# Optimization experiments

Hardware: AMD Instinct MI355X
Metric: run time of the kernel (lower is better)

## Reference

```python
import jax, jax.numpy as jnp
import numpy as np

N_DYADIC = 0  # dyadic refinement order 'n' from SigLoss_MMD.__init__


def _sig_gram(X, Y, n):
    """Gram matrix of signature kernels k(x_i, y_j) via the first-order
    finite-difference PDE scheme used by sig_kernels_f/fb_mmd:
        K[i+1,j+1] = K[i+1,j] + K[i,j+1] + K[i,j]*(<dx_i, dy_j> - 1)
    with dyadically refined increments dx = (x_{t+1}-x_t)/2^n repeated 2^n times.
    X: (A, M, D), Y: (B, N, D) -> returns (A, B) = K[:, :, -1, -1].
    The row recurrence is a cumulative sum, so each PDE row is one cumsum
    (fully vectorized over all (A,B) pairs); lax.scan runs over rows.
    """
    f = 2 ** n
    incX = jnp.repeat((X[:, 1:] - X[:, :-1]) / f, f, axis=1)  # (A, MM, D)
    incY = jnp.repeat((Y[:, 1:] - Y[:, :-1]) / f, f, axis=1)  # (B, NN, D)
    Mmat = jnp.einsum('aid,bjd->abij', incX, incY)            # (A, B, MM, NN)
    A, B, MM, NN = Mmat.shape
    ones_col = jnp.ones((A, B, 1), Mmat.dtype)
    row0 = jnp.ones((A, B, NN + 1), Mmat.dtype)               # K[0, :] = 1

    def step(prev_row, Mrow):  # prev_row: (A,B,NN+1), Mrow: (A,B,NN)
        # K[i+1,j+1] - K[i+1,j] = K[i,j+1] + K[i,j]*(M[i,j]-1)  -> cumsum
        inc = prev_row[..., 1:] + prev_row[..., :-1] * (Mrow - 1.0)
        new_row = jnp.concatenate([ones_col, 1.0 + jnp.cumsum(inc, axis=-1)], axis=-1)
        return new_row, None

    last_row, _ = jax.lax.scan(step, row0, jnp.moveaxis(Mmat, 2, 0))
    return last_row[..., -1]  # (A, B)


def setup_inputs() -> dict:
    key = jax.random.key(0)
    kx, ky = jax.random.split(key)
    A, M, D = 64, 128, 128
    SCALE = 0.025  # keeps increment inner products small so the PDE stays bounded
    X = SCALE * jax.random.normal(kx, (A, M, D), dtype=jnp.float32)
    Y = SCALE * jax.random.normal(ky, (A, M, D), dtype=jnp.float32)
    return {"X": X, "Y": Y}


def reference(X, Y):
    K_XX = _sig_gram(X, X, N_DYADIC)
    K_YY = _sig_gram(Y, Y, N_DYADIC)
    K_XY = _sig_gram(X, Y, N_DYADIC)
    mmd_squared = jnp.mean(K_XX) + jnp.mean(K_YY) - 2.0 * jnp.mean(K_XY)
    return mmd_squared
```

## Files before the change

### kernel.cpp

```cpp
#include <hip/hip_runtime.h>
#include <hip/hip_bf16.h>

#define MM 127
#define CHUNK_U16 4096
#define MAT_U16   16384
#define ARR_U16   1048576
#define QS_STRIDE 136
#define QS_DWORDS (64 * QS_STRIDE)

typedef __attribute__((ext_vector_type(8))) short short8;
typedef __attribute__((ext_vector_type(4))) float floatx4;

__device__ __forceinline__ unsigned short f2bf_rne(float x) {
  unsigned int u = __float_as_uint(x);
  u += 0x7FFFu + ((u >> 16) & 1u);
  return (unsigned short)(u >> 16);
}

__device__ __forceinline__ void gload_lds16(const void* g, void* l) {
  __builtin_amdgcn_global_load_lds(
      (const __attribute__((address_space(1))) unsigned int*)g,
      (__attribute__((address_space(3))) unsigned int*)l, 16, 0, 0);
}

__device__ __forceinline__ float wave_shr1(float x) {
  return __int_as_float(__builtin_amdgcn_update_dpp(
      0, __float_as_int(x), 0x138, 0xf, 0xf, true));
}

__global__ __launch_bounds__(256) void prep_kernel(
    const float* __restrict__ X, const float* __restrict__ Y,
    unsigned short* __restrict__ base, float* __restrict__ acc)
{
  if (blockIdx.x == 0 && threadIdx.x == 0) acc[0] = 0.f;
  const int bid = blockIdx.x;
  const int c = bid & 3;
  const int m = (bid >> 2) & 63;
  const int isY = bid >> 8;
  const float* src = (isY ? Y : X) + m * 128 * 128;
  unsigned short* dst = base + isY * ARR_U16 + m * MAT_U16 + c * CHUNK_U16;

  for (int s = threadIdx.x; s < 512; s += 256) {
    const int r = s >> 2;
    const int g = (s & 3) ^ (r & 3);
    uint4 hv = make_uint4(0, 0, 0, 0);
    if (r < MM) {
      const float* p = src + r * 128 + c * 32 + g * 8;
      float4 u0 = *reinterpret_cast<const float4*>(p);
      float4 u1 = *reinterpret_cast<const float4*>(p + 4);
      float4 v0 = *reinterpret_cast<const float4*>(p + 128);
      float4 v1 = *reinterpret_cast<const float4*>(p + 132);
      float d[8] = {v0.x - u0.x, v0.y - u0.y, v0.z - u0.z, v0.w - u0.w,
                    v1.x - u1.x, v1.y - u1.y, v1.z - u1.z, v1.w - u1.w};
      unsigned int hw[4];
#pragma unroll
      for (int e = 0; e < 4; ++e) {
        float2 rr; rr.x = d[2 * e]; rr.y = d[2 * e + 1];
        __hip_bfloat162 hp = __float22bfloat162_rn(rr);
        unsigned int hu; __builtin_memcpy(&hu, &hp, 4);
        hw[e] = hu;
      }
      hv = make_uint4(hw[0], hw[1], hw[2], hw[3]);
    }
    *reinterpret_cast<uint4*>(dst + s * 8) = hv;
  }
}

__global__ __launch_bounds__(256, 4) void sig_pair_kernel(
    const unsigned short* __restrict__ base, float* __restrict__ acc)
{
  __shared__ unsigned int smw[QS_DWORDS];
  unsigned short* const sm = reinterpret_cast<unsigned short*>(smw);
  const int tid = threadIdx.x;
  const int bid = blockIdx.x;

  float w;
  int a, b, srcA, srcB;
  if (bid < 4160) {
    int p = bid;
    srcA = 0;
    if (p >= 2080) { p -= 2080; srcA = 1; }
    srcB = srcA;
    int ia = (int)((sqrtf(8.0f * (float)p + 1.0f) - 1.0f) * 0.5f);
    while ((ia + 1) * (ia + 2) / 2 <= p) ia++;
    while (ia * (ia + 1) / 2 > p) ia--;
    int ib = p - ia * (ia + 1) / 2;
    a = ia; b = ib;
    w = (a == b ? 1.0f : 2.0f) / 4096.0f;
  } else {
    int p = bid - 4160;
    a = p >> 6; b = p & 63;
    srcA = 0; srcB = 1;
    w = -2.0f / 4096.0f;
  }
  const unsigned short* Am = base + srcA * ARR_U16 + a * MAT_U16;
  const unsigned short* Bm = base + srcB * ARR_U16 + b * MAT_U16;

  const int wid = tid >> 6, lane = tid & 63;
  const int row0 = (wid >> 1) * 64, col0 = (wid & 1) * 64;
  const int lrow = lane & 15, quad = lane >> 4;

  const unsigned short* gp = ((wid < 2) ? Am : Bm) + (wid & 1) * 2048 + lane * 8;
  const unsigned int dq = wid * 2048;

  floatx4 acc4[4][4];
#pragma unroll
  for (int tr = 0; tr < 4; ++tr)
#pragma unroll
    for (int tc = 0; tc < 4; ++tc) acc4[tr][tc] = (floatx4){0.f, 0.f, 0.f, 0.f};

#pragma unroll
  for (int s = 0; s < 4; ++s)
    gload_lds16(gp + s * 512, &sm[dq + s * 512]);

  for (int c = 0; c < 4; ++c) {
    __syncthreads();
    if (c < 3) {
      const unsigned short* g = gp + (c + 1) * CHUNK_U16;
      const unsigned int db_ = ((c + 1) & 1) * 8192 + dq;
#pragma unroll
      for (int s = 0; s < 4; ++s)
        gload_lds16(g + s * 512, &sm[db_ + s * 512]);
    }
    const unsigned int bb = (c & 1) * 8192;
    short8 bh[4];
#pragma unroll
    for (int tc = 0; tc < 4; ++tc) {
      int r = col0 + tc * 16 + lrow;
      int off = r * 32 + ((quad ^ (r & 3)) * 8);
      bh[tc] = *reinterpret_cast<const short8*>(&sm[bb + 4096 + off]);
    }
#pragma unroll
    for (int tr = 0; tr < 4; ++tr) {
      int r = row0 + tr * 16 + lrow;
      int off = r * 32 + ((quad ^ (r & 3)) * 8);
      short8 ah = *reinterpret_cast<const short8*>(&sm[bb + off]);
#pragma unroll
      for (int tc = 0; tc < 4; ++tc)
        acc4[tr][tc] = __builtin_amdgcn_mfma_f32_16x16x32_bf16(ah, bh[tc], acc4[tr][tc], 0, 0, 0);
    }
  }
  __syncthreads();

  for (int i = tid; i < QS_DWORDS; i += 256) smw[i] = 0u;
  __syncthreads();

#pragma unroll
  for (int tr = 0; tr < 4; ++tr) {
#pragma unroll
    for (int tc = 0; tc < 4; ++tc) {
      int jm = col0 + tc * 16 + lrow;
#pragma unroll
      for (int e = 0; e < 4; ++e) {
        int im = row0 + tr * 16 + quad * 4 + e;
        if (im < MM && jm < MM) {
          int lt = (jm + 1) >> 1;
          int phys = im + jm + 5 - 4 * (lt >> 1) - 4 * (lt & 1);
          int half = (jm & 1) ? 0 : 1;
          sm[(lt * QS_STRIDE + phys) * 2 + half] = f2bf_rne(acc4[tr][tc][e]);
        }
      }
    }
  }
  __syncthreads();

  if (wid == (bid & 3)) {
    const int l = lane;
    const int shift = 4 * (l >> 1) + 4 * (l & 1) - 4;
    const unsigned int lbase = l * QS_STRIDE;

    auto loadg = [&](int g) -> uint4 {
      int pb = 4 * g - shift;
      pb = pb < 0 ? 132 : (pb > 128 ? 128 : pb);
      return *reinterpret_cast<const uint4*>(&smw[lbase + pb]);
    };

    float curE = 1.f, curO = 1.f;
    float npE = (l == 0) ? 0.f : 1.f, npO = 1.f;
    uint4 P0 = loadg(0), P1 = loadg(1);

    for (int g = 0; g < 63; ++g) {
      const uint4 cur = P0;
      P0 = P1;
      if (g < 62) P1 = loadg(g + 2);
      unsigned int uu[4] = {cur.x, cur.y, cur.z, cur.w};
#pragma unroll
      for (int e = 0; e < 4; ++e) {
        unsigned int u = uu[e];
        float mE = __uint_as_float(u << 16) - 1.0f;
        float mO = __uint_as_float(u & 0xFFFF0000u) - 1.0f;
        float ncE = wave_shr1(curO);
        float ncO = curE;
        float vE = (curE + npE * mE) + ncE;
        float vO = (curO + npO * mO) + ncO;
        npE = ncE; npO = ncO;
        curE = vE; curO = vO;
      }
    }
    {
      unsigned int uu[2] = {P0.x, P0.y};
#pragma unroll
      for (int e = 0; e < 2; ++e) {
        unsigned int u = uu[e];
        float mE = __uint_as_float(u << 16) - 1.0f;
        float mO = __uint_as_float(u & 0xFFFF0000u) - 1.0f;
        float ncE = wave_shr1(curO);
        float ncO = curE;
        float vE = (curE + npE * mE) + ncE;
        float vO = (curO + npO * mO) + ncO;
        npE = ncE; npO = ncO;
        curE = vE; curO = vO;
      }
    }
    if (l == 63) atomicAdd(acc, w * curO);
  }
}

__global__ void finalize_kernel(const float* __restrict__ acc,
                                unsigned int* __restrict__ out) {
  float v = acc[0];
  __hip_bfloat16 bv = __float2bfloat16(v);
  unsigned short u;
  __builtin_memcpy(&u, &bv, sizeof(u));
  out[0] = ((unsigned int)u << 16) | (unsigned int)u;
}

extern "C" void kernel_launch(void* const* d_in, const int* in_sizes, int n_in,
                              void* d_out, int out_size, void* d_ws, size_t ws_size,
                              hipStream_t stream) {
  const float* X = (const float*)d_in[0];
  const float* Y = (const float*)d_in[1];
  float* acc = (float*)d_ws;
  unsigned short* base = (unsigned short*)((char*)d_ws + 1024);

  prep_kernel<<<512, 256, 0, stream>>>(X, Y, base, acc);
  sig_pair_kernel<<<8256, 256, 0, stream>>>(base, acc);
  finalize_kernel<<<1, 1, 0, stream>>>(acc, (unsigned int*)d_out);
}
```

Baseline: 202.8 us.

## Change LDS swizzle, vectorize scatter and zeroing, deepen recurrence prefetch

Changes the XOR swizzle for the bf16 increment tiles from (r&3) to ((r>>1)&3), in both the prep writer and the MFMA fragment reads, to cut LDS bank conflicts. It zeroes LDS with 16-byte stores, and packs pairs of accumulator values with a hardware bf16x2 conversion before scattering them into the skewed layout. The recurrence wave is now chosen from bits 8-9 of the block id instead of the low bits, and LDS prefetch for the recurrence deepens from two to three groups. Several unrelated micro-changes are mixed together. The extra prefetch register adds some register pressure.

```diff
diff --git a/kernel.cpp b/kernel.cpp
--- a/kernel.cpp
+++ b/kernel.cpp
@@ -11,10 +11,11 @@
 typedef __attribute__((ext_vector_type(8))) short short8;
 typedef __attribute__((ext_vector_type(4))) float floatx4;
 
-__device__ __forceinline__ unsigned short f2bf_rne(float x) {
-  unsigned int u = __float_as_uint(x);
-  u += 0x7FFFu + ((u >> 16) & 1u);
-  return (unsigned short)(u >> 16);
+__device__ __forceinline__ unsigned int pack_bf16_rne(float a, float b) {
+  float2 rr; rr.x = a; rr.y = b;
+  __hip_bfloat162 hp = __float22bfloat162_rn(rr);
+  unsigned int hu; __builtin_memcpy(&hu, &hp, 4);
+  return hu;
 }
 
 __device__ __forceinline__ void gload_lds16(const void* g, void* l) {
@@ -42,7 +43,7 @@
 
   for (int s = threadIdx.x; s < 512; s += 256) {
     const int r = s >> 2;
-    const int g = (s & 3) ^ (r & 3);
+    const int g = (s & 3) ^ ((r >> 1) & 3);
     uint4 hv = make_uint4(0, 0, 0, 0);
     if (r < MM) {
       const float* p = src + r * 128 + c * 32 + g * 8;
@@ -50,17 +51,10 @@
       float4 u1 = *reinterpret_cast<const float4*>(p + 4);
       float4 v0 = *reinterpret_cast<const float4*>(p + 128);
       float4 v1 = *reinterpret_cast<const float4*>(p + 132);
-      float d[8] = {v0.x - u0.x, v0.y - u0.y, v0.z - u0.z, v0.w - u0.w,
-                    v1.x - u1.x, v1.y - u1.y, v1.z - u1.z, v1.w - u1.w};
-      unsigned int hw[4];
-#pragma unroll
-      for (int e = 0; e < 4; ++e) {
-        float2 rr; rr.x = d[2 * e]; rr.y = d[2 * e + 1];
-        __hip_bfloat162 hp = __float22bfloat162_rn(rr);
-        unsigned int hu; __builtin_memcpy(&hu, &hp, 4);
-        hw[e] = hu;
-      }
-      hv = make_uint4(hw[0], hw[1], hw[2], hw[3]);
+      hv.x = pack_bf16_rne(v0.x - u0.x, v0.y - u0.y);
+      hv.y = pack_bf16_rne(v0.z - u0.z, v0.w - u0.w);
+      hv.z = pack_bf16_rne(v1.x - u1.x, v1.y - u1.y);
+      hv.w = pack_bf16_rne(v1.z - u1.z, v1.w - u1.w);
     }
     *reinterpret_cast<uint4*>(dst + s * 8) = hv;
   }
@@ -127,13 +121,13 @@
 #pragma unroll
     for (int tc = 0; tc < 4; ++tc) {
       int r = col0 + tc * 16 + lrow;
-      int off = r * 32 + ((quad ^ (r & 3)) * 8);
+      int off = r * 32 + ((quad ^ ((r >> 1) & 3)) * 8);
       bh[tc] = *reinterpret_cast<const short8*>(&sm[bb + 4096 + off]);
     }
 #pragma unroll
     for (int tr = 0; tr < 4; ++tr) {
       int r = row0 + tr * 16 + lrow;
-      int off = r * 32 + ((quad ^ (r & 3)) * 8);
+      int off = r * 32 + ((quad ^ ((r >> 1) & 3)) * 8);
       short8 ah = *reinterpret_cast<const short8*>(&sm[bb + off]);
 #pragma unroll
       for (int tc = 0; tc < 4; ++tc)
@@ -142,29 +136,36 @@
   }
   __syncthreads();
 
-  for (int i = tid; i < QS_DWORDS; i += 256) smw[i] = 0u;
+  {
+    uint4 z = make_uint4(0u, 0u, 0u, 0u);
+    uint4* smw4 = reinterpret_cast<uint4*>(smw);
+    for (int i = tid; i < QS_DWORDS / 4; i += 256) smw4[i] = z;
+  }
   __syncthreads();
 
 #pragma unroll
   for (int tr = 0; tr < 4; ++tr) {
+    const int im0 = row0 + tr * 16 + quad * 4;
 #pragma unroll
     for (int tc = 0; tc < 4; ++tc) {
-      int jm = col0 + tc * 16 + lrow;
-#pragma unroll
-      for (int e = 0; e < 4; ++e) {
-        int im = row0 + tr * 16 + quad * 4 + e;
-        if (im < MM && jm < MM) {
-          int lt = (jm + 1) >> 1;
-          int phys = im + jm + 5 - 4 * (lt >> 1) - 4 * (lt & 1);
-          int half = (jm & 1) ? 0 : 1;
-          sm[(lt * QS_STRIDE + phys) * 2 + half] = f2bf_rne(acc4[tr][tc][e]);
-        }
+      const int jm = col0 + tc * 16 + lrow;
+      if (jm < MM) {
+        const int lt = (jm + 1) >> 1;
+        const int half = (jm & 1) ? 0 : 1;
+        const int phys0 = im0 + jm + 5 - 4 * (lt >> 1) - 4 * (lt & 1);
+        unsigned short* p = &sm[(lt * QS_STRIDE + phys0) * 2 + half];
+        unsigned int u01 = pack_bf16_rne(acc4[tr][tc][0], acc4[tr][tc][1]);
+        unsigned int u23 = pack_bf16_rne(acc4[tr][tc][2], acc4[tr][tc][3]);
+        p[0] = (unsigned short)u01;
+        p[2] = (unsigned short)(u01 >> 16);
+        p[4] = (unsigned short)u23;
+        if (im0 + 3 < MM) p[6] = (unsigned short)(u23 >> 16);
       }
     }
   }
   __syncthreads();
 
-  if (wid == (bid & 3)) {
+  if (wid == ((bid >> 8) & 3)) {
     const int l = lane;
     const int shift = 4 * (l >> 1) + 4 * (l & 1) - 4;
     const unsigned int lbase = l * QS_STRIDE;
@@ -177,12 +178,12 @@
 
     float curE = 1.f, curO = 1.f;
     float npE = (l == 0) ? 0.f : 1.f, npO = 1.f;
-    uint4 P0 = loadg(0), P1 = loadg(1);
+    uint4 P0 = loadg(0), P1 = loadg(1), P2 = loadg(2);
 
     for (int g = 0; g < 63; ++g) {
       const uint4 cur = P0;
-      P0 = P1;
-      if (g < 62) P1 = loadg(g + 2);
+      P0 = P1; P1 = P2;
+      if (g < 61) P2 = loadg(g + 3);
       unsigned int uu[4] = {cur.x, cur.y, cur.z, cur.w};
 #pragma unroll
       for (int e = 0; e < 4; ++e) {
```

Result: faster. 187.3 us (-7.6%).
